# Kernel tuning notes

Measured on AMD Instinct MI355X. Metric: run time of the kernel, lower is better.

Reference implementation:

```python
import jax, jax.numpy as jnp
import numpy as np

NEG = -1e30  # stand-in for -inf that keeps logaddexp grad-safe


def _ctc_neg_log_likelihood(predictions, labels):
    # predictions: [B, T, C] logits; labels: [B, L] int, -1 = padding.
    # tf.nn.ctc_loss(blank_index=-1) => blank class is C-1.
    B, T, C = predictions.shape
    L = labels.shape[1]
    S = 2 * L + 1
    blank = C - 1

    label_len = jnp.sum((labels != -1).astype(jnp.int32), axis=-1)  # [B]
    labels_c = jnp.where(labels < 0, 0, labels).astype(jnp.int32)

    # Extended label sequence: blank, l1, blank, l2, ..., blank  -> [B, S]
    ext = jnp.full((B, S), blank, dtype=jnp.int32)
    ext = ext.at[:, 1::2].set(labels_c)

    # s-2 transition allowed only at label positions (odd s) with ext[s] != ext[s-2]
    same = jnp.concatenate([jnp.zeros((B, 2), bool), ext[:, 2:] == ext[:, :-2]], axis=1)
    is_label_pos = (jnp.arange(S) % 2 == 1)[None, :]
    allow2 = is_label_pos & ~same  # [B, S]

    # valid extended positions per example: s < 2*label_len + 1
    valid = jnp.arange(S)[None, :] < (2 * label_len + 1)[:, None]  # [B, S]

    log_probs = jax.nn.log_softmax(predictions, axis=-1)  # [B, T, C]
    # emission log-prob for each extended-label slot: [B, T, S]
    lp_ext = jnp.take_along_axis(log_probs, jnp.broadcast_to(ext[:, None, :], (B, T, S)), axis=2)

    has_lab = label_len > 0
    alpha0 = jnp.full((B, S), NEG, dtype=log_probs.dtype)
    alpha0 = alpha0.at[:, 0].set(lp_ext[:, 0, 0])
    alpha0 = alpha0.at[:, 1].set(jnp.where(has_lab, lp_ext[:, 0, 1], NEG))
    alpha0 = jnp.where(valid, alpha0, NEG)

    def step(alpha, lp_t):
        a1 = alpha
        a2 = jnp.pad(alpha, ((0, 0), (1, 0)), constant_values=NEG)[:, :S]
        a3 = jnp.pad(alpha, ((0, 0), (2, 0)), constant_values=NEG)[:, :S]
        a3 = jnp.where(allow2, a3, NEG)
        new = jnp.logaddexp(jnp.logaddexp(a1, a2), a3) + lp_t
        new = jnp.where(valid, new, NEG)
        return new, None

    lp_rest = jnp.moveaxis(lp_ext[:, 1:], 1, 0)  # [T-1, B, S]
    alphaT, _ = jax.lax.scan(step, alpha0, lp_rest)

    idx1 = (2 * label_len)[:, None]              # final blank
    idx2 = jnp.maximum(idx1 - 1, 0)              # final label
    a_end1 = jnp.take_along_axis(alphaT, idx1, axis=1)[:, 0]
    a_end2 = jnp.take_along_axis(alphaT, idx2, axis=1)[:, 0]
    a_end2 = jnp.where(has_lab, a_end2, NEG)
    log_lik = jnp.logaddexp(a_end1, a_end2)
    return -log_lik  # [B]


def setup_inputs() -> dict:
    key = jax.random.key(0)
    k1, k2 = jax.random.split(key)
    B, T, C, L = 1024, 384, 96, 48
    labels = jax.random.randint(k1, (B, L), 0, C - 1).astype(jnp.int64)
    predictions = jax.random.normal(k2, (B, T, C), dtype=jnp.float32)
    return {"labels": labels, "predictions": predictions}


def reference(labels, predictions):
    per_example = _ctc_neg_log_likelihood(predictions, labels)
    return jnp.mean(per_example)
```

## Files before the change

### kernel.cpp

```cpp
#include <hip/hip_runtime.h>

constexpr int Tt = 384;
constexpr int Cc = 96;
constexpr int Ll = 48;
constexpr int Gg = 8;
constexpr int NG = 24;

#define L2E 1.4426950408889634f
#define LN2 0.6931471805599453f
#define LNEG (-3.0e38f)

template <int CTRL, int RM = 0xF>
__device__ __forceinline__ float dppf(float x) {
    return __int_as_float(
        __builtin_amdgcn_update_dpp(0, __float_as_int(x), CTRL, RM, 0xF, true));
}
template <int CTRL>
__device__ __forceinline__ int dppi(int x) {
    return __builtin_amdgcn_update_dpp(0, x, CTRL, 0xF, 0xF, true);
}
__device__ __forceinline__ float bcast63(float x) {
    return __int_as_float(__builtin_amdgcn_readlane(__float_as_int(x), 63));
}
__device__ __forceinline__ float wsum(float x) {
    x += dppf<0x111>(x);
    x += dppf<0x112>(x);
    x += dppf<0x114>(x);
    x += dppf<0x118>(x);
    x += dppf<0x142, 0xA>(x);
    x += dppf<0x143, 0xC>(x);
    return bcast63(x);
}
__device__ __forceinline__ float shup1(float x) { return dppf<0x138>(x); }
__device__ __forceinline__ float shdn1(float x) { return dppf<0x130>(x); }
__device__ __forceinline__ float exp2i(int d) {
    d = d < -126 ? -126 : (d > 126 ? 126 : d);
    return __int_as_float((d + 127) << 23);
}

template <bool FWD>
__device__ __forceinline__ void prod_load(const float2* __restrict__ rp2, float2* q,
                                          int g, int lane) {
#pragma unroll
    for (int j = 0; j < Gg; ++j) {
        int k = g * Gg + j;
        int t = FWD ? k : (Tt - 1 - k);
        q[j] = (lane < 48) ? rp2[(size_t)t * 48 + lane] : make_float2(-1e4f, -1e4f);
    }
}

__device__ __forceinline__ void gather_group(const float2* q, float* el, float* eb,
                                             int idx_h, int bitsel, double& zacc) {
#pragma unroll
    for (int j = 0; j < Gg; ++j) {
        float ex = __builtin_amdgcn_exp2f(q[j].x * L2E);
        float ey = __builtin_amdgcn_exp2f(q[j].y * L2E);
        float gb = __shfl(ey, 47, 64);
        float g0 = __shfl(ex, idx_h, 64);
        float g1 = __shfl(ey, idx_h, 64);
        el[j] = bitsel ? g1 : g0;
        eb[j] = gb;
        float s = wsum(ex + ey);
        zacc += (double)__log2f(s);
    }
}

template <bool FWD>
__device__ __forceinline__ void dp_group(const float* el, const float* eb,
                                         float allow2f, float& st_e, float& st_o,
                                         int& ls, float& f, float& a2f) {
#pragma unroll
    for (int j = 0; j < Gg; ++j) {
        if (FWD) {
            float sh = shup1(st_o);
            float t0 = st_e + st_o;
            float ne = fmaf(f, sh, st_e) * eb[j];
            float no = fmaf(a2f, sh, t0) * el[j];
            st_e = ne; st_o = no;
        } else {
            float en = shdn1(st_e);
            float on = shdn1(st_o);
            float ne = (st_e + st_o) * eb[j];
            float no = fmaf(a2f, on, fmaf(f, en, st_o)) * el[j];
            st_e = ne; st_o = no;
        }
    }
    float m = fmaxf(st_e, st_o);
    bool z  = (m == 0.0f);
    int eb2 = (__float_as_int(m) >> 23) & 0xFF;
    eb2 = eb2 > 253 ? 253 : eb2;
    float r = z ? 1.0f : __int_as_float((254 - eb2) << 23);
    st_e *= r; st_o *= r;
    ls += z ? 0 : (eb2 - 127);
#pragma unroll
    for (int it = 0; it < 8; ++it) {
        int lsn = FWD ? dppi<0x138>(ls) : dppi<0x130>(ls);
        ls = z ? lsn : ls;
    }
    int lsn2 = FWD ? dppi<0x138>(ls) : dppi<0x130>(ls);
    f   = exp2i(lsn2 - ls);
    a2f = allow2f * f;
}

template <bool FWD>
__device__ __forceinline__ void run_half(const float2* __restrict__ rp2, int lane,
                                         int idx_h, int bitsel, float allow2f,
                                         float& st_e, float& st_o, int& ls,
                                         float& f, float& a2f, double& zacc) {
    float2 q0[Gg], q1[Gg];
    float elA[Gg], ebA[Gg], elB[Gg], ebB[Gg];
    prod_load<FWD>(rp2, q0, 0, lane);
    prod_load<FWD>(rp2, q1, 1, lane);
    gather_group(q0, elA, ebA, idx_h, bitsel, zacc);
    for (int g2 = 0; g2 < NG / 2; ++g2) {
        bool more = (g2 < NG / 2 - 1);
        if (more) prod_load<FWD>(rp2, q0, 2 * g2 + 2, lane);
        gather_group(q1, elB, ebB, idx_h, bitsel, zacc);
        dp_group<FWD>(elA, ebA, allow2f, st_e, st_o, ls, f, a2f);
        if (more) prod_load<FWD>(rp2, q1, 2 * g2 + 3, lane);
        if (more) gather_group(q0, elA, ebA, idx_h, bitsel, zacc);
        dp_group<FWD>(elB, ebB, allow2f, st_e, st_o, ls, f, a2f);
    }
}

__global__ __launch_bounds__(128) void ctc_fb(const int* __restrict__ labels,
                                              const float* __restrict__ pred,
                                              float* __restrict__ nll) {
    const int b    = blockIdx.x;
    const int lane = threadIdx.x & 63;
    const int wv   = threadIdx.x >> 6;
    const float2* rp2 = (const float2*)(pred + (size_t)b * Tt * Cc);

    __shared__ float  sbe[64], sbo[64];
    __shared__ int    slsb[64];
    __shared__ double szb;

    int v = (lane < Ll) ? labels[(size_t)b * Ll + lane] : -1;
    int present = (lane < Ll) && (v != -1);
    int labv = (v < 0) ? 0 : v;
    unsigned long long pm = __ballot(present);
    int len = __popcll(pm);
    int idx_h  = labv >> 1;
    int bitsel = labv & 1;
    int lab_p = __shfl(labv, (lane - 1) & 63, 64);
    int lab_n = __shfl(labv, (lane + 1) & 63, 64);

    float st_e, st_o = 0.0f, f = 1.0f, a2f, allow2f;
    int   ls = 0;
    double zacc = 0.0;

    if (wv == 0) {
        allow2f = (lane >= 1 && labv != lab_p) ? 1.0f : 0.0f;
        st_e = (lane == 0) ? 1.0f : 0.0f;
        a2f = allow2f;
        run_half<true>(rp2, lane, idx_h, bitsel, allow2f, st_e, st_o, ls, f, a2f, zacc);
    } else {
        allow2f = (labv != lab_n) ? 1.0f : 0.0f;
        st_e = (lane == len) ? 1.0f : 0.0f;
        a2f = allow2f;
        run_half<false>(rp2, lane, idx_h, bitsel, allow2f, st_e, st_o, ls, f, a2f, zacc);
        sbe[lane]  = st_e;
        sbo[lane]  = st_o;
        slsb[lane] = ls;
        if (lane == 0) szb = zacc;
    }
    __syncthreads();

    if (wv == 0) {
        float sh  = shup1(st_o);
        int   lsu = dppi<0x138>(ls);
        float fup = exp2i(lsu - ls);
        float Ae = fmaf(fup, sh, st_e);
        float Ao = fmaf(allow2f * fup, sh, st_e + st_o);
        float be = sbe[lane], bo = sbo[lane];
        float base = (float)(ls + slsb[lane]);
        float l1 = (Ae > 0.0f && be > 0.0f) ? __log2f(Ae) + __log2f(be) + base : LNEG;
        float l2 = (Ao > 0.0f && bo > 0.0f) ? __log2f(Ao) + __log2f(bo) + base : LNEG;
        float mm = fmaxf(l1, l2);
#pragma unroll
        for (int off = 32; off >= 1; off >>= 1) mm = fmaxf(mm, __shfl_xor(mm, off, 64));
        float ss = exp2f(l1 - mm) + exp2f(l2 - mm);
#pragma unroll
        for (int off = 32; off >= 1; off >>= 1) ss += __shfl_xor(ss, off, 64);
        if (lane == 0) {
            double zt = zacc + szb;
            float ll = (mm + __log2f(ss) - (float)zt) * LN2;
            nll[b] = -ll;
        }
    }
}

__global__ __launch_bounds__(256) void ctc_mean(const float* __restrict__ nll,
                                                float* __restrict__ out, float invB) {
    __shared__ double part[256];
    double s = 0.0;
#pragma unroll
    for (int i = 0; i < 4; ++i) s += (double)nll[threadIdx.x + 256 * i];
    part[threadIdx.x] = s;
    __syncthreads();
#pragma unroll
    for (int w = 128; w >= 1; w >>= 1) {
        if (threadIdx.x < w) part[threadIdx.x] += part[threadIdx.x + w];
        __syncthreads();
    }
    if (threadIdx.x == 0) out[0] = (float)(part[0] * (double)invB);
}

extern "C" void kernel_launch(void* const* d_in, const int* in_sizes, int n_in,
                              void* d_out, int out_size, void* d_ws, size_t ws_size,
                              hipStream_t stream) {
    const int*   labels = (const int*)d_in[0];
    const float* pred   = (const float*)d_in[1];
    float*       out    = (float*)d_out;
    float*       nll    = (float*)d_ws;

    const int B = in_sizes[0] / Ll;

    hipLaunchKernelGGL(ctc_fb, dim3(B), dim3(128), 0, stream, labels, pred, nll);
    hipLaunchKernelGGL(ctc_mean, dim3(1), dim3(256), 0, stream, nll, out, 1.0f / (float)B);
}
```

Before: 220.0 us.

## Stage prediction rows into an LDS ring via async global_load_lds

Replaces register double-buffered global loads with a 6-slot LDS ring filled by global_load_lds (direct global-to-LDS DMA), waiting with vmcnt so several groups of timesteps are in flight ahead of the DP recurrence. Each lane then reads its float2 from LDS, and padding lanes are masked in the softmax sum instead of at load time. This aims to hide global memory latency behind the serial forward/backward recurrence without holding large register buffers. It adds about 37 KB of LDS per block, which may reduce occupancy, and correctness depends on the hand-written waitcnt values matching the number of outstanding loads.

```diff
diff --git a/kernel.cpp b/kernel.cpp
--- a/kernel.cpp
+++ b/kernel.cpp
@@ -5,10 +5,16 @@
 constexpr int Ll = 48;
 constexpr int Gg = 8;
 constexpr int NG = 24;
+constexpr int RSLOTS = 6;
+constexpr int SLOTB  = Gg * Cc * 4;
+constexpr int RINGB  = RSLOTS * SLOTB + 512;
 
 #define L2E 1.4426950408889634f
 #define LN2 0.6931471805599453f
 #define LNEG (-3.0e38f)
+
+typedef __attribute__((address_space(3))) void       lds_t;
+typedef const __attribute__((address_space(1))) void gmem_t;
 
 template <int CTRL, int RM = 0xF>
 __device__ __forceinline__ float dppf(float x) {
@@ -39,28 +45,33 @@
 }
 
 template <bool FWD>
-__device__ __forceinline__ void prod_load(const float2* __restrict__ rp2, float2* q,
-                                          int g, int lane) {
+__device__ __forceinline__ void stage_group(const float* __restrict__ rp, char* slot,
+                                            int g, int lane) {
+    const int t0 = FWD ? (8 * g) : (376 - 8 * g);
+    const char* src = (const char*)(rp + (size_t)t0 * Cc);
+#pragma unroll
+    for (int c = 0; c < 3; ++c) {
+        __builtin_amdgcn_global_load_lds((gmem_t*)(src + c * 1024 + lane * 16),
+                                         (lds_t*)(slot + c * 1024), 16, 0, 0);
+    }
+}
+
+template <bool FWD>
+__device__ __forceinline__ void consume_group(const char* slot, int lane,
+                                              int idx_h, int bitsel, double& zacc,
+                                              float* el, float* eb) {
 #pragma unroll
     for (int j = 0; j < Gg; ++j) {
-        int k = g * Gg + j;
-        int t = FWD ? k : (Tt - 1 - k);
-        q[j] = (lane < 48) ? rp2[(size_t)t * 48 + lane] : make_float2(-1e4f, -1e4f);
-    }
-}
-
-__device__ __forceinline__ void gather_group(const float2* q, float* el, float* eb,
-                                             int idx_h, int bitsel, double& zacc) {
-#pragma unroll
-    for (int j = 0; j < Gg; ++j) {
-        float ex = __builtin_amdgcn_exp2f(q[j].x * L2E);
-        float ey = __builtin_amdgcn_exp2f(q[j].y * L2E);
+        const int off = FWD ? j : (7 - j);
+        float2 q = *(const float2*)(slot + off * 384 + lane * 8);
+        float ex = __builtin_amdgcn_exp2f(q.x * L2E);
+        float ey = __builtin_amdgcn_exp2f(q.y * L2E);
         float gb = __shfl(ey, 47, 64);
         float g0 = __shfl(ex, idx_h, 64);
         float g1 = __shfl(ey, idx_h, 64);
         el[j] = bitsel ? g1 : g0;
         eb[j] = gb;
-        float s = wsum(ex + ey);
+        float s = wsum((lane < 48) ? (ex + ey) : 0.0f);
         zacc += (double)__log2f(s);
     }
 }
@@ -103,23 +114,23 @@
 }
 
 template <bool FWD>
-__device__ __forceinline__ void run_half(const float2* __restrict__ rp2, int lane,
-                                         int idx_h, int bitsel, float allow2f,
-                                         float& st_e, float& st_o, int& ls,
-                                         float& f, float& a2f, double& zacc) {
-    float2 q0[Gg], q1[Gg];
-    float elA[Gg], ebA[Gg], elB[Gg], ebB[Gg];
-    prod_load<FWD>(rp2, q0, 0, lane);
-    prod_load<FWD>(rp2, q1, 1, lane);
-    gather_group(q0, elA, ebA, idx_h, bitsel, zacc);
-    for (int g2 = 0; g2 < NG / 2; ++g2) {
-        bool more = (g2 < NG / 2 - 1);
-        if (more) prod_load<FWD>(rp2, q0, 2 * g2 + 2, lane);
-        gather_group(q1, elB, ebB, idx_h, bitsel, zacc);
-        dp_group<FWD>(elA, ebA, allow2f, st_e, st_o, ls, f, a2f);
-        if (more) prod_load<FWD>(rp2, q1, 2 * g2 + 3, lane);
-        if (more) gather_group(q0, elA, ebA, idx_h, bitsel, zacc);
-        dp_group<FWD>(elB, ebB, allow2f, st_e, st_o, ls, f, a2f);
+__device__ __forceinline__ void run_half(const float* __restrict__ rp, char* ring,
+                                         int lane, int idx_h, int bitsel,
+                                         float allow2f, float& st_e, float& st_o,
+                                         int& ls, float& f, float& a2f, double& zacc) {
+#pragma unroll
+    for (int g = 0; g < RSLOTS; ++g)
+        stage_group<FWD>(rp, ring + g * SLOTB, g, lane);
+    float el[Gg], eb[Gg];
+    for (int g = 0; g < NG; ++g) {
+        asm volatile("s_waitcnt vmcnt(15)" ::: "memory");
+        __builtin_amdgcn_sched_barrier(0);
+        consume_group<FWD>(ring + (g % RSLOTS) * SLOTB, lane, idx_h, bitsel, zacc, el, eb);
+        dp_group<FWD>(el, eb, allow2f, st_e, st_o, ls, f, a2f);
+        __builtin_amdgcn_sched_barrier(0);
+        asm volatile("s_waitcnt lgkmcnt(0)" ::: "memory");
+        if (g + RSLOTS < NG)
+            stage_group<FWD>(rp, ring + (g % RSLOTS) * SLOTB, g + RSLOTS, lane);
     }
 }
 
@@ -129,8 +140,9 @@
     const int b    = blockIdx.x;
     const int lane = threadIdx.x & 63;
     const int wv   = threadIdx.x >> 6;
-    const float2* rp2 = (const float2*)(pred + (size_t)b * Tt * Cc);
-
+    const float* rp = pred + (size_t)b * Tt * Cc;
+
+    __shared__ __align__(16) char ring[2][RINGB];
     __shared__ float  sbe[64], sbo[64];
     __shared__ int    slsb[64];
     __shared__ double szb;
@@ -153,12 +165,14 @@
         allow2f = (lane >= 1 && labv != lab_p) ? 1.0f : 0.0f;
         st_e = (lane == 0) ? 1.0f : 0.0f;
         a2f = allow2f;
-        run_half<true>(rp2, lane, idx_h, bitsel, allow2f, st_e, st_o, ls, f, a2f, zacc);
+        run_half<true>(rp, ring[0], lane, idx_h, bitsel, allow2f,
+                       st_e, st_o, ls, f, a2f, zacc);
     } else {
         allow2f = (labv != lab_n) ? 1.0f : 0.0f;
         st_e = (lane == len) ? 1.0f : 0.0f;
         a2f = allow2f;
-        run_half<false>(rp2, lane, idx_h, bitsel, allow2f, st_e, st_o, ls, f, a2f, zacc);
+        run_half<false>(rp, ring[1], lane, idx_h, bitsel, allow2f,
+                        st_e, st_o, ls, f, a2f, zacc);
         sbe[lane]  = st_e;
         sbo[lane]  = st_o;
         slsb[lane] = ls;
```

After: 227.8 us. +3.6%, slower.
